# Kernel tuning notes

Hardware: AMD Instinct MI355X
Metric: run time of the kernel (lower is better)

## Reference

```python
import jax, jax.numpy as jnp
import numpy as np

WS = 7      # window size
SS = 3      # shift size = WS // 2
NH = 12     # num heads
EPS = 1e-5  # LayerNorm eps


def _ln(x, g, b):
    m = jnp.mean(x, axis=-1, keepdims=True)
    v = jnp.var(x, axis=-1, keepdims=True)
    return (x - m) * jax.lax.rsqrt(v + EPS) * g + b


def _rel_index(ws):
    # relative position index (N, N), N = ws*ws (static, numpy)
    coords = np.stack(np.meshgrid(np.arange(ws), np.arange(ws), indexing='ij')).reshape(2, -1)
    rel = (coords[:, :, None] - coords[:, None, :]).transpose(1, 2, 0).copy()
    rel[:, :, 0] += ws - 1
    rel[:, :, 1] += ws - 1
    rel[:, :, 0] *= 2 * ws - 1
    return rel.sum(-1)


def _attn_mask(H, W, ws, ss):
    # SW-MSA mask (nW, N, N): -100 where tokens come from different shifted regions
    img = np.zeros((H, W), np.float32)
    cnt = 0
    sls = (slice(0, -ws), slice(-ws, -ss), slice(-ss, None))
    for hs in sls:
        for wsl in sls:
            img[hs, wsl] = cnt
            cnt += 1
    win = img.reshape(H // ws, ws, W // ws, ws).transpose(0, 2, 1, 3).reshape(-1, ws * ws)
    d = win[:, None, :] - win[:, :, None]
    return np.where(d != 0, -100.0, 0.0).astype(np.float32)


def _forward(x, rel_bias_table, qkv_w, qkv_b, proj_w, proj_b,
             norm1_w, norm1_b, norm2_w, norm2_b,
             mlp_w1, mlp_b1, mlp_w2, mlp_b2, h, w):
    B, L, C = x.shape
    ws, ss, nH = WS, SS, NH
    hd = C // nH
    N = ws * ws
    scale = hd ** -0.5
    nWh, nWw = h // ws, w // ws
    nW = nWh * nWw

    shortcut = x
    y = _ln(x, norm1_w, norm1_b).reshape(B, h, w, C)
    # cyclic shift (SW-MSA)
    y = jnp.roll(y, (-ss, -ss), axis=(1, 2))
    # window partition -> (B*nW, N, C)
    y = y.reshape(B, nWh, ws, nWw, ws, C).transpose(0, 1, 3, 2, 4, 5).reshape(-1, N, C)

    qkv = (y @ qkv_w + qkv_b).reshape(-1, N, 3, nH, hd).transpose(2, 0, 3, 1, 4)
    q, k, v = qkv[0] * scale, qkv[1], qkv[2]  # (Bw, nH, N, hd)

    attn = jnp.einsum('bhnd,bhmd->bhnm', q, k)  # (Bw, nH, N, N)
    # learned relative position bias
    idx = jnp.asarray(_rel_index(ws))  # (N, N)
    bias = rel_bias_table[idx].transpose(2, 0, 1)[None]  # (1, nH, N, N)
    attn = attn + bias
    # shifted-window mask
    mask = jnp.asarray(_attn_mask(h, w, ws, ss))  # (nW, N, N)
    attn = attn.reshape(B, nW, nH, N, N) + mask[None, :, None]
    attn = jax.nn.softmax(attn.reshape(-1, nH, N, N), axis=-1)

    out = jnp.einsum('bhnm,bhmd->bhnd', attn, v).transpose(0, 2, 1, 3).reshape(-1, N, C)
    out = out @ proj_w + proj_b
    # window reverse + un-shift
    out = out.reshape(B, nWh, nWw, ws, ws, C).transpose(0, 1, 3, 2, 4, 5).reshape(B, h, w, C)
    out = jnp.roll(out, (ss, ss), axis=(1, 2)).reshape(B, L, C)

    x = shortcut + out
    y2 = _ln(x, norm2_w, norm2_b)
    mlp = jax.nn.gelu(y2 @ mlp_w1 + mlp_b1, approximate=False) @ mlp_w2 + mlp_b2
    return x + mlp


def setup_inputs() -> dict:
    key = jax.random.key(0)
    ks = jax.random.split(key, 8)
    B, H, W, C = 32, 56, 56, 384
    hid = int(C * 4.0)
    ws, nH = WS, NH
    inp = {
        'x': jax.random.normal(ks[0], (B, H * W, C), jnp.float32),
        'rel_bias_table': 0.02 * jax.random.normal(ks[1], ((2 * ws - 1) * (2 * ws - 1), nH), jnp.float32),
        'qkv_w': 0.02 * jax.random.normal(ks[2], (C, 3 * C), jnp.float32),
        'qkv_b': jnp.zeros((3 * C,), jnp.float32),
        'proj_w': 0.02 * jax.random.normal(ks[3], (C, C), jnp.float32),
        'proj_b': jnp.zeros((C,), jnp.float32),
        'norm1_w': jnp.ones((C,), jnp.float32),
        'norm1_b': jnp.zeros((C,), jnp.float32),
        'norm2_w': jnp.ones((C,), jnp.float32),
        'norm2_b': jnp.zeros((C,), jnp.float32),
        'mlp_w1': 0.02 * jax.random.normal(ks[4], (C, hid), jnp.float32),
        'mlp_b1': jnp.zeros((hid,), jnp.float32),
        'mlp_w2': 0.02 * jax.random.normal(ks[5], (hid, C), jnp.float32),
        'mlp_b2': jnp.zeros((C,), jnp.float32),
        'h': H,
        'w': W,
    }
    return inp


def reference(x, rel_bias_table, qkv_w, qkv_b, proj_w, proj_b,
              norm1_w, norm1_b, norm2_w, norm2_b,
              mlp_w1, mlp_b1, mlp_w2, mlp_b2, h, w):
    return _forward(x, rel_bias_table, qkv_w, qkv_b, proj_w, proj_b,
                    norm1_w, norm1_b, norm2_w, norm2_b,
                    mlp_w1, mlp_b1, mlp_w2, mlp_b2, h, w)
```

## Files before the change

### kernel.cpp

```cpp
#include <hip/hip_runtime.h>

typedef unsigned short u16;
typedef unsigned int u32;
typedef short s8v __attribute__((ext_vector_type(8)));
typedef float f4 __attribute__((ext_vector_type(4)));

#define GL16(g, l) __builtin_amdgcn_global_load_lds((const __attribute__((address_space(1))) u32*)(g), (__attribute__((address_space(3))) u32*)(l), 16, 0, 0)

__device__ __forceinline__ u16 f2bf(float f){
  u32 u = __builtin_bit_cast(u32, f);
  u32 r = u + 0x7fffu + ((u >> 16) & 1u);
  return (u16)(r >> 16);
}
__device__ __forceinline__ float bf2f(u16 u){
  u32 x = ((u32)u) << 16;
  return __builtin_bit_cast(float, x);
}

__device__ __forceinline__ u32 pk_bf16(float lo, float hi){
  u32 r;
  asm("v_cvt_pk_bf16_f32 %0, %1, %2" : "=v"(r) : "v"(lo), "v"(hi));
  return r;
}

__device__ __forceinline__ float gelu_f(float x){
  float y = fabsf(x) * 0.70710678118654752f;
  float t = __builtin_amdgcn_rcpf(1.f + 0.3275911f*y);
  float p = ((((1.061405429f*t - 1.453152027f)*t + 1.421413741f)*t - 0.284496736f)*t + 0.254829592f)*t;
  float er = 1.f - p*__expf(-y*y);
  er = copysignf(er, x);
  return 0.5f*x*(1.f + er);
}

__device__ __forceinline__ int win_to_src(int orow){
  int wi = orow / 49;
  int n  = orow - wi*49;
  int b  = wi >> 6;
  int wq = wi & 63;
  int wh = wq >> 3, ww = wq & 7;
  int r = n / 7, c = n - r*7;
  int hh = wh*7 + r + 3; if (hh >= 56) hh -= 56;
  int wp = ww*7 + c + 3; if (wp >= 56) wp -= 56;
  return (b*56 + hh)*56 + wp;
}

__global__ void sentinel_kernel(float* o){ o[0] = 1.0e9f; }

__global__ void transpose_cast(const float* __restrict__ in, u16* __restrict__ out,
                               int K, int N, float scale, int scale_lim){
  __shared__ float tile[16][17];
  int kb = blockIdx.x*16, nb = blockIdx.y*16;
  int tx = threadIdx.x, ty = threadIdx.y;
  int k = kb + ty, n = nb + tx;
  tile[ty][tx] = (k < K && n < N) ? in[(size_t)k*N + n] : 0.f;
  __syncthreads();
  int on = nb + ty, ok = kb + tx;
  if (on < N && ok < K){
    float v = tile[tx][ty];
    if (on < scale_lim) v *= scale;
    out[(size_t)on*K + ok] = f2bf(v);
  }
}

__global__ void scale_bias(const float* __restrict__ in, float* __restrict__ out,
                           int n, float s, int lim){
  int i = blockIdx.x*256 + threadIdx.x;
  if (i < n) out[i] = in[i] * (i < lim ? s : 1.f);
}

__global__ void build_biasmask(const float* __restrict__ table, u16* __restrict__ bm){
  int wq = blockIdx.x, h = blockIdx.y;
  int wh = wq >> 3, ww = wq & 7;
  u16* o = bm + (size_t)(wq*12 + h) * 4096;
  for (int i = threadIdx.x; i < 4096; i += 256){
    int m = i >> 6, n = i & 63;
    float v;
    if (m < 49 && n < 49){
      int rm = m/7, cm = m - rm*7;
      int rn = n/7, cn = n - rn*7;
      int idx = (rm - rn + 6)*13 + (cm - cn + 6);
      v = table[idx*12 + h];
      int ym = wh*7 + rm, xm = ww*7 + cm;
      int yn = wh*7 + rn, xn = ww*7 + cn;
      int lm = (ym < 49 ? 0 : (ym < 53 ? 1 : 2))*3 + (xm < 49 ? 0 : (xm < 53 ? 1 : 2));
      int ln = (yn < 49 ? 0 : (yn < 53 ? 1 : 2))*3 + (xn < 49 ? 0 : (xn < 53 ? 1 : 2));
      if (lm != ln) v += -100.f;
    } else {
      v = -1e9f;
    }
    o[i] = f2bf(v);
  }
}

template<bool GATHER>
__global__ __launch_bounds__(256) void ln_kernel(const float* __restrict__ x,
    const float* __restrict__ g, const float* __restrict__ b,
    u16* __restrict__ y, int nrows)
{
  int row = blockIdx.x*4 + (threadIdx.x >> 6);
  int lane = threadIdx.x & 63;
  if (row >= nrows) return;
  int src = GATHER ? win_to_src(row) : row;
  const float* xr = x + (size_t)src*384;
  float v[6];
  float s = 0.f, s2 = 0.f;
  #pragma unroll
  for (int p = 0; p < 3; p++){
    float2 t = *(const float2*)(xr + p*128 + lane*2);
    v[p*2] = t.x; v[p*2+1] = t.y;
    s += t.x + t.y; s2 += t.x*t.x + t.y*t.y;
  }
  #pragma unroll
  for (int off = 32; off; off >>= 1){
    s  += __shfl_xor(s,  off);
    s2 += __shfl_xor(s2, off);
  }
  float mean = s * (1.f/384.f);
  float var  = s2 * (1.f/384.f) - mean*mean;
  float rs   = rsqrtf(var + 1e-5f);
  u16* yr = y + (size_t)row*384;
  #pragma unroll
  for (int p = 0; p < 3; p++){
    int c = p*128 + lane*2;
    float a0 = (v[p*2]   - mean)*rs*g[c]   + b[c];
    float a1 = (v[p*2+1] - mean)*rs*g[c+1] + b[c+1];
    *(u32*)(yr + c) = pk_bf16(a0, a1);
  }
}

template<int MODE>
__global__ __launch_bounds__(512, 4) void gemm_bf16(
    const u16* __restrict__ A, const u16* __restrict__ Bt,
    const float* __restrict__ bias, const float* __restrict__ resid,
    void* __restrict__ outp, int K, int N, int gn)
{
  __shared__ u16 smem[36864];
  const int tid  = threadIdx.x;
  const int lane = tid & 63, wv = tid >> 6;
  const int wm = wv >> 1, wn = wv & 1;
  const int l15 = lane & 15, lhi = lane >> 4;
  const int key = (l15 >> 1) & 3;

  int total = gridDim.x;
  int flat  = blockIdx.x;
  int swz   = flat;
  if ((total & 7) == 0){
    int cpx = total >> 3;
    swz = (flat & 7)*cpx + (flat >> 3);
  }
  int bm = swz / gn, bn = swz - bm*gn;
  const size_t m0 = (size_t)bm * 256;
  const int n0 = bn * 128;

  f4 acc[4][4] = {};

  const int c0 = tid, c1 = 512 + tid;
  const u16* sA0 = A + (m0 + (size_t)(c0 >> 2))*K + ((c0 & 3) ^ ((c0 >> 3) & 3))*8;
  const u16* sA1 = A + (m0 + (size_t)(c1 >> 2))*K + ((c1 & 3) ^ ((c1 >> 3) & 3))*8;
  const u16* sB0 = Bt + ((size_t)n0 + (c0 >> 2))*K + ((c0 & 3) ^ ((c0 >> 3) & 3))*8;
  const int dA0 = (0   + wv*64)*8, dA1 = (512 + wv*64)*8;
  const int dB0 = dA0;

  int aoff[4], boff[4];
  #pragma unroll
  for (int mi = 0; mi < 4; mi++)
    aoff[mi] = (wm*64 + mi*16 + l15)*32 + (lhi ^ key)*8;
  #pragma unroll
  for (int ni = 0; ni < 4; ni++)
    boff[ni] = (wn*64 + ni*16 + l15)*32 + (lhi ^ key)*8;

  const int nk = K >> 5;

  GL16(sA0, &smem[0*8192 + dA0]); GL16(sA1, &smem[0*8192 + dA1]);
  GL16(sB0, &smem[24576 + 0*4096 + dB0]);
  GL16(sA0+32, &smem[1*8192 + dA0]); GL16(sA1+32, &smem[1*8192 + dA1]);
  GL16(sB0+32, &smem[24576 + 1*4096 + dB0]);
  sA0 += 64; sA1 += 64; sB0 += 64;

  int kt = 0;
  #define KSTEP(BUF_CUR, BUF_N2)                                               \
  {                                                                            \
    if (kt + 1 < nk) { asm volatile("s_waitcnt vmcnt(3)" ::: "memory"); }      \
    else             { asm volatile("s_waitcnt vmcnt(0)" ::: "memory"); }      \
    asm volatile("s_waitcnt lgkmcnt(0)" ::: "memory");                         \
    __builtin_amdgcn_s_barrier();                                              \
    if (kt + 2 < nk){                                                          \
      GL16(sA0, &smem[(BUF_N2)*8192 + dA0]);                                   \
      GL16(sA1, &smem[(BUF_N2)*8192 + dA1]);                                   \
      GL16(sB0, &smem[24576 + (BUF_N2)*4096 + dB0]);                           \
      sA0 += 32; sA1 += 32; sB0 += 32;                                         \
    }                                                                          \
    s8v a[4], bb[4];                                                           \
    _Pragma("unroll")                                                          \
    for (int mi = 0; mi < 4; mi++)                                             \
      a[mi] = *(const s8v*)&smem[(BUF_CUR)*8192 + aoff[mi]];                   \
    _Pragma("unroll")                                                          \
    for (int ni = 0; ni < 4; ni++)                                             \
      bb[ni] = *(const s8v*)&smem[24576 + (BUF_CUR)*4096 + boff[ni]];          \
    __builtin_amdgcn_s_setprio(1);                                             \
    _Pragma("unroll")                                                          \
    for (int mi = 0; mi < 4; mi++)                                             \
      _Pragma("unroll")                                                        \
      for (int ni = 0; ni < 4; ni++)                                           \
        acc[mi][ni] = __builtin_amdgcn_mfma_f32_16x16x32_bf16(                 \
            bb[ni], a[mi], acc[mi][ni], 0, 0, 0);                              \
    __builtin_amdgcn_s_setprio(0);                                             \
    kt++;                                                                      \
  }

  const int nIter = nk / 3;
  for (int it3 = 0; it3 < nIter; it3++){
    KSTEP(0, 2)
    KSTEP(1, 0)
    KSTEP(2, 1)
  }
  #undef KSTEP

  if constexpr (MODE == 0 || MODE == 2){
    asm volatile("s_waitcnt lgkmcnt(0)" ::: "memory");
    __builtin_amdgcn_s_barrier();
    u16* tile = smem;
    #pragma unroll
    for (int mi = 0; mi < 4; mi++){
      int ml = wm*64 + mi*16 + l15;
      #pragma unroll
      for (int ni = 0; ni < 4; ni++){
        int nl = wn*64 + ni*16 + lhi*4;
        f4 v = acc[mi][ni];
        float4 b4 = *(const float4*)(bias + n0 + nl);
        v[0] += b4.x; v[1] += b4.y; v[2] += b4.z; v[3] += b4.w;
        u32 p0, p1;
        if constexpr (MODE == 2){
          p0 = pk_bf16(gelu_f(v[0]), gelu_f(v[1]));
          p1 = pk_bf16(gelu_f(v[2]), gelu_f(v[3]));
        } else {
          p0 = pk_bf16(v[0], v[1]);
          p1 = pk_bf16(v[2], v[3]);
        }
        *(u32*)&tile[ml*136 + nl]     = p0;
        *(u32*)&tile[ml*136 + nl + 2] = p1;
      }
    }
    __syncthreads();
    int rr = tid >> 4;
    int cc = (tid & 15) * 8;
    #pragma unroll
    for (int pass = 0; pass < 8; pass++){
      int row = rr + pass*32;
      uint4 val = *(const uint4*)&tile[row*136 + cc];
      *(uint4*)((u16*)outp + ((size_t)((int)m0 + row))*N + n0 + cc) = val;
    }
  } else {
    #pragma unroll
    for (int mi = 0; mi < 4; mi++){
      int m = (int)m0 + wm*64 + mi*16 + l15;
      int src = 0;
      if constexpr (MODE == 1) src = win_to_src(m);
      #pragma unroll
      for (int ni = 0; ni < 4; ni++){
        int n = n0 + wn*64 + ni*16 + lhi*4;
        f4 v = acc[mi][ni];
        float4 b4 = *(const float4*)(bias + n);
        v[0] += b4.x; v[1] += b4.y; v[2] += b4.z; v[3] += b4.w;
        if constexpr (MODE == 1){
          const float4 r4 = *(const float4*)(resid + (size_t)src*384 + n);
          float4 o4; o4.x = v[0]+r4.x; o4.y = v[1]+r4.y; o4.z = v[2]+r4.z; o4.w = v[3]+r4.w;
          *(float4*)((float*)outp + (size_t)src*384 + n) = o4;
        } else {
          float4* o = (float4*)((float*)outp + (size_t)m*N + n);
          float4 c4 = *o;
          c4.x += v[0]; c4.y += v[1]; c4.z += v[2]; c4.w += v[3];
          *o = c4;
        }
      }
    }
  }
}

__global__ __launch_bounds__(256) void attn_kernel(
    const u16* __restrict__ qkv, const u16* __restrict__ bm, u16* __restrict__ ao)
{
  const int wi = blockIdx.x;
  const int hg = blockIdx.y;
  const int wv = threadIdx.x >> 6, lane = threadIdx.x & 63;
  const int h = hg*4 + wv;
  const int l15 = lane & 15, lhi = lane >> 4;
  const int wq = wi & 63;

  __shared__ u16 Plds[4][64*72];
  __shared__ u16 Vlds[4][32*72];

  const size_t base = (size_t)wi * 49 * 1152;
  s8v z8 = (s8v)0;

  #pragma unroll
  for (int i = 0; i < 4; i++){
    int n  = i*16 + (lane >> 2);
    int d8 = (lane & 3)*8;
    s8v v = (n < 49) ? *(const s8v*)&qkv[base + (size_t)n*1152 + 768 + h*32 + d8] : z8;
    #pragma unroll
    for (int j = 0; j < 8; j++)
      Vlds[wv][(d8 + j)*72 + n] = (u16)v[j];
  }

  s8v aQ[4], bK[4];
  #pragma unroll
  for (int mi = 0; mi < 4; mi++){
    int rowq = mi*16 + l15;
    aQ[mi] = (rowq < 49) ? *(const s8v*)&qkv[base + (size_t)rowq*1152 +   0 + h*32 + lhi*8] : z8;
    bK[mi] = (rowq < 49) ? *(const s8v*)&qkv[base + (size_t)rowq*1152 + 384 + h*32 + lhi*8] : z8;
  }
  f4 zf = {0.f, 0.f, 0.f, 0.f};
  f4 s[4][4];
  __builtin_amdgcn_s_setprio(1);
  #pragma unroll
  for (int mi = 0; mi < 4; mi++)
    #pragma unroll
    for (int ni = 0; ni < 4; ni++)
      s[mi][ni] = __builtin_amdgcn_mfma_f32_16x16x32_bf16(aQ[mi], bK[ni], zf, 0, 0, 0);
  __builtin_amdgcn_s_setprio(0);

  const u16* bmp = bm + (size_t)(wq*12 + h) * 4096;
  #pragma unroll
  for (int mi = 0; mi < 4; mi++)
    #pragma unroll
    for (int ni = 0; ni < 4; ni++)
      #pragma unroll
      for (int r = 0; r < 4; r++){
        int m = mi*16 + lhi*4 + r, n = ni*16 + l15;
        s[mi][ni][r] += bf2f(bmp[m*64 + n]);
      }

  #pragma unroll
  for (int mi = 0; mi < 4; mi++){
    #pragma unroll
    for (int r = 0; r < 4; r++){
      float mx = fmaxf(fmaxf(s[mi][0][r], s[mi][1][r]), fmaxf(s[mi][2][r], s[mi][3][r]));
      mx = fmaxf(mx, __shfl_xor(mx, 1));
      mx = fmaxf(mx, __shfl_xor(mx, 2));
      mx = fmaxf(mx, __shfl_xor(mx, 4));
      mx = fmaxf(mx, __shfl_xor(mx, 8));
      float sum = 0.f;
      #pragma unroll
      for (int ni = 0; ni < 4; ni++){
        float p = __expf(s[mi][ni][r] - mx);
        s[mi][ni][r] = p; sum += p;
      }
      sum += __shfl_xor(sum, 1);
      sum += __shfl_xor(sum, 2);
      sum += __shfl_xor(sum, 4);
      sum += __shfl_xor(sum, 8);
      float inv = 1.f / sum;
      #pragma unroll
      for (int ni = 0; ni < 4; ni++) s[mi][ni][r] *= inv;
    }
  }

  #pragma unroll
  for (int mi = 0; mi < 4; mi++)
    #pragma unroll
    for (int ni = 0; ni < 4; ni++)
      #pragma unroll
      for (int r = 0; r < 4; r++){
        int m = mi*16 + lhi*4 + r, n = ni*16 + l15;
        Plds[wv][m*72 + n] = f2bf(s[mi][ni][r]);
      }
  __syncthreads();

  f4 o[4][2] = {};
  #pragma unroll
  for (int ks = 0; ks < 2; ks++){
    s8v aP[4], bV[2];
    #pragma unroll
    for (int mi = 0; mi < 4; mi++)
      aP[mi] = *(const s8v*)&Plds[wv][(mi*16 + l15)*72 + ks*32 + lhi*8];
    #pragma unroll
    for (int di = 0; di < 2; di++)
      bV[di] = *(const s8v*)&Vlds[wv][(di*16 + l15)*72 + ks*32 + lhi*8];
    __builtin_amdgcn_s_setprio(1);
    #pragma unroll
    for (int mi = 0; mi < 4; mi++)
      #pragma unroll
      for (int di = 0; di < 2; di++)
        o[mi][di] = __builtin_amdgcn_mfma_f32_16x16x32_bf16(aP[mi], bV[di], o[mi][di], 0, 0, 0);
    __builtin_amdgcn_s_setprio(0);
  }

  #pragma unroll
  for (int mi = 0; mi < 4; mi++)
    #pragma unroll
    for (int di = 0; di < 2; di++)
      #pragma unroll
      for (int r = 0; r < 4; r++){
        int m = mi*16 + lhi*4 + r;
        if (m < 49){
          int d = di*16 + l15;
          ao[((size_t)wi*49 + m)*384 + h*32 + d] = f2bf(o[mi][di][r]);
        }
      }
}

extern "C" void kernel_launch(void* const* d_in, const int* in_sizes, int n_in,
                              void* d_out, int out_size, void* d_ws, size_t ws_size,
                              hipStream_t stream)
{
  const float* x      = (const float*)d_in[0];
  const float* table  = (const float*)d_in[1];
  const float* qkv_w  = (const float*)d_in[2];
  const float* qkv_b  = (const float*)d_in[3];
  const float* proj_w = (const float*)d_in[4];
  const float* proj_b = (const float*)d_in[5];
  const float* n1w    = (const float*)d_in[6];
  const float* n1b    = (const float*)d_in[7];
  const float* n2w    = (const float*)d_in[8];
  const float* n2b    = (const float*)d_in[9];
  const float* w1     = (const float*)d_in[10];
  const float* b1     = (const float*)d_in[11];
  const float* w2     = (const float*)d_in[12];
  const float* b2     = (const float*)d_in[13];
  float* out = (float*)d_out;

  const size_t M = 100352;
  const float SC = 0.17677669529663689f;

  const size_t R1 = M * 1536 * 2;
  const size_t R2 = M * 384 * 2;
  const size_t R3 = (size_t)64*12*64*64*2;
  const size_t WT = (size_t)(1152*384 + 384*384 + 1536*384 + 384*1536) * 2;
  const size_t BB = 1152 * 4;
  const size_t needed = R1 + R2 + R3 + WT + BB;
  if (ws_size < needed){
    sentinel_kernel<<<1, 1, 0, stream>>>(out);
    return;
  }

  char* p = (char*)d_ws;
  u16*   qkvbuf = (u16*)p;
  u16*   ybuf   = (u16*)(p + R1);
  u16*   bmbuf  = (u16*)(p + R1 + R2);
  u16*   qkvT   = (u16*)(p + R1 + R2 + R3);
  u16*   projT  = qkvT  + (size_t)1152*384;
  u16*   w1T    = projT + (size_t)384*384;
  u16*   w2T    = w1T   + (size_t)1536*384;
  float* qkvb_s = (float*)(p + R1 + R2 + R3 + WT);

  transpose_cast<<<dim3(24, 72),  dim3(16,16), 0, stream>>>(qkv_w,  qkvT, 384, 1152, SC, 384);
  transpose_cast<<<dim3(24, 24),  dim3(16,16), 0, stream>>>(proj_w, projT, 384, 384, 1.f, 0);
  transpose_cast<<<dim3(24, 96),  dim3(16,16), 0, stream>>>(w1,     w1T,  384, 1536, 1.f, 0);
  transpose_cast<<<dim3(96, 24),  dim3(16,16), 0, stream>>>(w2,     w2T,  1536, 384, 1.f, 0);
  scale_bias<<<5, 256, 0, stream>>>(qkv_b, qkvb_s, 1152, SC, 384);
  build_biasmask<<<dim3(64, 12), 256, 0, stream>>>(table, bmbuf);

  ln_kernel<true><<<M/4, 256, 0, stream>>>(x, n1w, n1b, ybuf, (int)M);

  gemm_bf16<0><<<392*9, 512, 0, stream>>>(ybuf, qkvT, qkvb_s, nullptr, qkvbuf, 384, 1152, 9);

  attn_kernel<<<dim3(2048, 3), 256, 0, stream>>>(qkvbuf, bmbuf, ybuf);

  gemm_bf16<1><<<392*3, 512, 0, stream>>>(ybuf, projT, proj_b, x, out, 384, 384, 3);

  ln_kernel<false><<<M/4, 256, 0, stream>>>(out, n2w, n2b, ybuf, (int)M);

  gemm_bf16<2><<<392*12, 512, 0, stream>>>(ybuf, w1T, b1, nullptr, qkvbuf, 384, 1536, 12);

  gemm_bf16<3><<<392*3, 512, 0, stream>>>(qkvbuf, w2T, b2, nullptr, out, 1536, 384, 3);
}
```

Before: 874.5 us.

## Fuse MLP fc1+GELU+fc2 into one kernel keeping hidden activations in LDS

Replaces the separate fc1 (GELU, bf16 hidden write) and fc2 (accumulate into output) GEMM launches with a single fused kernel per 128-row tile. The A tile is loaded once into LDS, hidden chunks of 64 columns are computed, passed through GELU and staged in swizzled LDS, then immediately consumed by fc2 into register accumulators. This removes the round trip of the large hidden tensor through global memory and one launch. In exchange, weights are read straight from global memory without LDS staging, the grid is much smaller with heavy register use, and each hidden chunk needs a barrier, so per-block latency and occupancy may suffer.

```diff
diff --git a/kernel.cpp b/kernel.cpp
--- a/kernel.cpp
+++ b/kernel.cpp
@@ -216,7 +216,7 @@
   }
   #undef KSTEP
 
-  if constexpr (MODE == 0 || MODE == 2){
+  if constexpr (MODE == 0){
     asm volatile("s_waitcnt lgkmcnt(0)" ::: "memory");
     __builtin_amdgcn_s_barrier();
     u16* tile = smem;
@@ -229,14 +229,8 @@
         f4 v = acc[mi][ni];
         float4 b4 = *(const float4*)(bias + n0 + nl);
         v[0] += b4.x; v[1] += b4.y; v[2] += b4.z; v[3] += b4.w;
-        u32 p0, p1;
-        if constexpr (MODE == 2){
-          p0 = pk_bf16(gelu_f(v[0]), gelu_f(v[1]));
-          p1 = pk_bf16(gelu_f(v[2]), gelu_f(v[3]));
-        } else {
-          p0 = pk_bf16(v[0], v[1]);
-          p1 = pk_bf16(v[2], v[3]);
-        }
+        u32 p0 = pk_bf16(v[0], v[1]);
+        u32 p1 = pk_bf16(v[2], v[3]);
         *(u32*)&tile[ml*136 + nl]     = p0;
         *(u32*)&tile[ml*136 + nl + 2] = p1;
       }
@@ -254,25 +248,136 @@
     #pragma unroll
     for (int mi = 0; mi < 4; mi++){
       int m = (int)m0 + wm*64 + mi*16 + l15;
-      int src = 0;
-      if constexpr (MODE == 1) src = win_to_src(m);
+      int src = win_to_src(m);
       #pragma unroll
       for (int ni = 0; ni < 4; ni++){
         int n = n0 + wn*64 + ni*16 + lhi*4;
         f4 v = acc[mi][ni];
         float4 b4 = *(const float4*)(bias + n);
-        v[0] += b4.x; v[1] += b4.y; v[2] += b4.z; v[3] += b4.w;
-        if constexpr (MODE == 1){
-          const float4 r4 = *(const float4*)(resid + (size_t)src*384 + n);
-          float4 o4; o4.x = v[0]+r4.x; o4.y = v[1]+r4.y; o4.z = v[2]+r4.z; o4.w = v[3]+r4.w;
-          *(float4*)((float*)outp + (size_t)src*384 + n) = o4;
-        } else {
-          float4* o = (float4*)((float*)outp + (size_t)m*N + n);
-          float4 c4 = *o;
-          c4.x += v[0]; c4.y += v[1]; c4.z += v[2]; c4.w += v[3];
-          *o = c4;
-        }
-      }
+        const float4 r4 = *(const float4*)(resid + (size_t)src*384 + n);
+        float4 o4; o4.x = v[0]+b4.x+r4.x; o4.y = v[1]+b4.y+r4.y;
+        o4.z = v[2]+b4.z+r4.z; o4.w = v[3]+b4.w+r4.w;
+        *(float4*)((float*)outp + (size_t)src*384 + n) = o4;
+      }
+    }
+  }
+}
+
+__global__ __launch_bounds__(512, 2) void fused_mlp(
+    const u16* __restrict__ A, const u16* __restrict__ w1T,
+    const u16* __restrict__ w2T, const float* __restrict__ b1,
+    const float* __restrict__ b2, float* __restrict__ outp)
+{
+  __shared__ u16 smem[65536];
+  const int tid = threadIdx.x;
+  const int lane = tid & 63, wv = tid >> 6;
+  const int wm = wv >> 2, wn = wv & 3;
+  const int wm1 = wv & 3, wn1 = wv >> 2;
+  const int l15 = lane & 15, lhi = lane >> 4;
+
+  int total = gridDim.x, flat = blockIdx.x, swz = flat;
+  if ((total & 7) == 0){ int cpx = total >> 3; swz = (flat & 7)*cpx + (flat >> 3); }
+  const size_t m0 = (size_t)swz * 128;
+
+  #pragma unroll
+  for (int it = 0; it < 12; it++){
+    int idx = it*512 + tid;
+    int row = idx / 48, g = idx - row*48;
+    const u16* gp = A + (m0 + (size_t)row)*384 + (size_t)(g ^ (row & 7))*8;
+    GL16(gp, &smem[(it*512 + wv*64)*8]);
+  }
+  asm volatile("s_waitcnt vmcnt(0)" ::: "memory");
+  __builtin_amdgcn_s_barrier();
+
+  f4 oacc[4][6] = {};
+
+  auto chunk = [&](int hbase, u16* Hc){
+    f4 acc1[2][2] = {};
+    #pragma unroll
+    for (int ks = 0; ks < 12; ks++){
+      s8v wf[2], af[2];
+      #pragma unroll
+      for (int nj = 0; nj < 2; nj++){
+        int n = hbase + wn1*32 + nj*16 + l15;
+        wf[nj] = *(const s8v*)&w1T[(size_t)n*384 + ks*32 + lhi*8];
+      }
+      #pragma unroll
+      for (int mi = 0; mi < 2; mi++){
+        int m = wm1*32 + mi*16 + l15;
+        int gk = (ks*4 + lhi) ^ (m & 7);
+        af[mi] = *(const s8v*)&smem[m*384 + gk*8];
+      }
+      __builtin_amdgcn_s_setprio(1);
+      #pragma unroll
+      for (int mi = 0; mi < 2; mi++)
+        #pragma unroll
+        for (int nj = 0; nj < 2; nj++)
+          acc1[mi][nj] = __builtin_amdgcn_mfma_f32_16x16x32_bf16(
+              wf[nj], af[mi], acc1[mi][nj], 0, 0, 0);
+      __builtin_amdgcn_s_setprio(0);
+    }
+    #pragma unroll
+    for (int mi = 0; mi < 2; mi++){
+      int m = wm1*32 + mi*16 + l15;
+      #pragma unroll
+      for (int nj = 0; nj < 2; nj++){
+        int h = wn1*32 + nj*16 + lhi*4;
+        f4 v = acc1[mi][nj];
+        float4 b4 = *(const float4*)(b1 + hbase + h);
+        v[0]+=b4.x; v[1]+=b4.y; v[2]+=b4.z; v[3]+=b4.w;
+        u32 p0 = pk_bf16(gelu_f(v[0]), gelu_f(v[1]));
+        u32 p1 = pk_bf16(gelu_f(v[2]), gelu_f(v[3]));
+        int gh = (h >> 3) ^ (m & 7);
+        u32* dst = (u32*)&Hc[m*64 + gh*8 + (h & 7)];
+        dst[0] = p0; dst[1] = p1;
+      }
+    }
+    asm volatile("s_waitcnt lgkmcnt(0)" ::: "memory");
+    __builtin_amdgcn_s_barrier();
+
+    #pragma unroll
+    for (int ks = 0; ks < 2; ks++){
+      s8v a2[4], w2f[6];
+      #pragma unroll
+      for (int nj = 0; nj < 6; nj++){
+        int n = wn*96 + nj*16 + l15;
+        w2f[nj] = *(const s8v*)&w2T[(size_t)n*1536 + hbase + ks*32 + lhi*8];
+      }
+      #pragma unroll
+      for (int mi = 0; mi < 4; mi++){
+        int m = wm*64 + mi*16 + l15;
+        int gk = (ks*4 + lhi) ^ (m & 7);
+        a2[mi] = *(const s8v*)&Hc[m*64 + gk*8];
+      }
+      __builtin_amdgcn_s_setprio(1);
+      #pragma unroll
+      for (int mi = 0; mi < 4; mi++)
+        #pragma unroll
+        for (int nj = 0; nj < 6; nj++)
+          oacc[mi][nj] = __builtin_amdgcn_mfma_f32_16x16x32_bf16(
+              w2f[nj], a2[mi], oacc[mi][nj], 0, 0, 0);
+      __builtin_amdgcn_s_setprio(0);
+    }
+  };
+
+  for (int hp = 0; hp < 12; hp++){
+    chunk(hp*128,      &smem[49152]);
+    chunk(hp*128 + 64, &smem[57344]);
+  }
+
+  #pragma unroll
+  for (int mi = 0; mi < 4; mi++){
+    int m = (int)m0 + wm*64 + mi*16 + l15;
+    #pragma unroll
+    for (int nj = 0; nj < 6; nj++){
+      int n = wn*96 + nj*16 + lhi*4;
+      f4 v = oacc[mi][nj];
+      float4 b4 = *(const float4*)(b2 + n);
+      float4* o = (float4*)(outp + (size_t)m*384 + n);
+      float4 c4 = *o;
+      c4.x += v[0]+b4.x; c4.y += v[1]+b4.y;
+      c4.z += v[2]+b4.z; c4.w += v[3]+b4.w;
+      *o = c4;
     }
   }
 }
@@ -461,7 +566,5 @@
 
   ln_kernel<false><<<M/4, 256, 0, stream>>>(out, n2w, n2b, ybuf, (int)M);
 
-  gemm_bf16<2><<<392*12, 512, 0, stream>>>(ybuf, w1T, b1, nullptr, qkvbuf, 384, 1536, 12);
-
-  gemm_bf16<3><<<392*3, 512, 0, stream>>>(qkvbuf, w2T, b2, nullptr, out, 1536, 384, 3);
-}
+  fused_mlp<<<784, 512, 0, stream>>>(ybuf, w1T, w2T, b1, b2, out);
+}
```

Result: slower. 1.450 ms (+65.9%).

## Specialize GEMM warps into dedicated load producers and MFMA consumers

Applied to the files above, without the earlier changes.

Adds two producer wavefronts per GEMM block (640 threads) that issue all global-to-LDS loads, while the eight original wavefronts only read LDS and run MFMAs. This aims to take load issue and address arithmetic off the compute waves so loads overlap better with matrix math. It raises threads per block and register pressure under a tighter launch bound (640,5). Producers wait on vmcnt(12) while consumers wait on lgkmcnt, so correctness depends on barrier ordering with the global_load_lds path.

```diff
diff --git a/kernel.cpp b/kernel.cpp
--- a/kernel.cpp
+++ b/kernel.cpp
@@ -129,7 +129,7 @@
 }
 
 template<int MODE>
-__global__ __launch_bounds__(512, 4) void gemm_bf16(
+__global__ __launch_bounds__(640, 5) void gemm_bf16(
     const u16* __restrict__ A, const u16* __restrict__ Bt,
     const float* __restrict__ bias, const float* __restrict__ resid,
     void* __restrict__ outp, int K, int N, int gn)
@@ -137,6 +137,7 @@
   __shared__ u16 smem[36864];
   const int tid  = threadIdx.x;
   const int lane = tid & 63, wv = tid >> 6;
+  const bool producer = (wv >= 8);
   const int wm = wv >> 1, wn = wv & 1;
   const int l15 = lane & 15, lhi = lane >> 4;
   const int key = (l15 >> 1) & 3;
@@ -154,12 +155,39 @@
 
   f4 acc[4][4] = {};
 
-  const int c0 = tid, c1 = 512 + tid;
-  const u16* sA0 = A + (m0 + (size_t)(c0 >> 2))*K + ((c0 & 3) ^ ((c0 >> 3) & 3))*8;
-  const u16* sA1 = A + (m0 + (size_t)(c1 >> 2))*K + ((c1 & 3) ^ ((c1 >> 3) & 3))*8;
-  const u16* sB0 = Bt + ((size_t)n0 + (c0 >> 2))*K + ((c0 & 3) ^ ((c0 >> 3) & 3))*8;
-  const int dA0 = (0   + wv*64)*8, dA1 = (512 + wv*64)*8;
-  const int dB0 = dA0;
+  const int p = wv - 8;
+  const u16* spA[8]; const u16* spB[4];
+  int dA[8], dB[4];
+  if (producer){
+    #pragma unroll
+    for (int it = 0; it < 8; it++){
+      int c = (it*2 + p)*64 + lane;
+      int row = c >> 2;
+      int col = ((c & 3) ^ ((c >> 3) & 3)) * 8;
+      spA[it] = A + (m0 + (size_t)row)*K + col;
+      dA[it] = (it*2 + p)*512;
+    }
+    #pragma unroll
+    for (int it = 0; it < 4; it++){
+      int c = (it*2 + p)*64 + lane;
+      int row = c >> 2;
+      int col = ((c & 3) ^ ((c >> 3) & 3)) * 8;
+      spB[it] = Bt + ((size_t)n0 + row)*K + col;
+      dB[it] = (it*2 + p)*512;
+    }
+  }
+
+  #define STAGEP(BUF)                                                          \
+  {                                                                            \
+    _Pragma("unroll")                                                          \
+    for (int it = 0; it < 8; it++) GL16(spA[it], &smem[(BUF)*8192 + dA[it]]);  \
+    _Pragma("unroll")                                                          \
+    for (int it = 0; it < 4; it++) GL16(spB[it], &smem[24576 + (BUF)*4096 + dB[it]]); \
+    _Pragma("unroll")                                                          \
+    for (int it = 0; it < 8; it++) spA[it] += 32;                              \
+    _Pragma("unroll")                                                          \
+    for (int it = 0; it < 4; it++) spB[it] += 32;                              \
+  }
 
   int aoff[4], boff[4];
   #pragma unroll
@@ -171,40 +199,40 @@
 
   const int nk = K >> 5;
 
-  GL16(sA0, &smem[0*8192 + dA0]); GL16(sA1, &smem[0*8192 + dA1]);
-  GL16(sB0, &smem[24576 + 0*4096 + dB0]);
-  GL16(sA0+32, &smem[1*8192 + dA0]); GL16(sA1+32, &smem[1*8192 + dA1]);
-  GL16(sB0+32, &smem[24576 + 1*4096 + dB0]);
-  sA0 += 64; sA1 += 64; sB0 += 64;
+  if (producer){
+    STAGEP(0)
+    STAGEP(1)
+  }
 
   int kt = 0;
   #define KSTEP(BUF_CUR, BUF_N2)                                               \
   {                                                                            \
-    if (kt + 1 < nk) { asm volatile("s_waitcnt vmcnt(3)" ::: "memory"); }      \
-    else             { asm volatile("s_waitcnt vmcnt(0)" ::: "memory"); }      \
-    asm volatile("s_waitcnt lgkmcnt(0)" ::: "memory");                         \
+    if (producer){                                                             \
+      if (kt + 1 < nk) { asm volatile("s_waitcnt vmcnt(12)" ::: "memory"); }   \
+      else             { asm volatile("s_waitcnt vmcnt(0)" ::: "memory"); }    \
+    } else {                                                                   \
+      asm volatile("s_waitcnt lgkmcnt(0)" ::: "memory");                       \
+    }                                                                          \
     __builtin_amdgcn_s_barrier();                                              \
-    if (kt + 2 < nk){                                                          \
-      GL16(sA0, &smem[(BUF_N2)*8192 + dA0]);                                   \
-      GL16(sA1, &smem[(BUF_N2)*8192 + dA1]);                                   \
-      GL16(sB0, &smem[24576 + (BUF_N2)*4096 + dB0]);                           \
-      sA0 += 32; sA1 += 32; sB0 += 32;                                         \
-    }                                                                          \
-    s8v a[4], bb[4];                                                           \
-    _Pragma("unroll")                                                          \
-    for (int mi = 0; mi < 4; mi++)                                             \
-      a[mi] = *(const s8v*)&smem[(BUF_CUR)*8192 + aoff[mi]];                   \
-    _Pragma("unroll")                                                          \
-    for (int ni = 0; ni < 4; ni++)                                             \
-      bb[ni] = *(const s8v*)&smem[24576 + (BUF_CUR)*4096 + boff[ni]];          \
-    __builtin_amdgcn_s_setprio(1);                                             \
-    _Pragma("unroll")                                                          \
-    for (int mi = 0; mi < 4; mi++)                                             \
+    if (producer){                                                             \
+      if (kt + 2 < nk){ STAGEP(BUF_N2) }                                       \
+    } else {                                                                   \
+      s8v a[4], bb[4];                                                         \
+      _Pragma("unroll")                                                        \
+      for (int mi = 0; mi < 4; mi++)                                           \
+        a[mi] = *(const s8v*)&smem[(BUF_CUR)*8192 + aoff[mi]];                 \
       _Pragma("unroll")                                                        \
       for (int ni = 0; ni < 4; ni++)                                           \
-        acc[mi][ni] = __builtin_amdgcn_mfma_f32_16x16x32_bf16(                 \
-            bb[ni], a[mi], acc[mi][ni], 0, 0, 0);                              \
-    __builtin_amdgcn_s_setprio(0);                                             \
+        bb[ni] = *(const s8v*)&smem[24576 + (BUF_CUR)*4096 + boff[ni]];        \
+      __builtin_amdgcn_s_setprio(1);                                           \
+      _Pragma("unroll")                                                        \
+      for (int mi = 0; mi < 4; mi++)                                           \
+        _Pragma("unroll")                                                      \
+        for (int ni = 0; ni < 4; ni++)                                         \
+          acc[mi][ni] = __builtin_amdgcn_mfma_f32_16x16x32_bf16(               \
+              bb[ni], a[mi], acc[mi][ni], 0, 0, 0);                            \
+      __builtin_amdgcn_s_setprio(0);                                           \
+    }                                                                          \
     kt++;                                                                      \
   }
 
@@ -215,62 +243,69 @@
     KSTEP(2, 1)
   }
   #undef KSTEP
+  #undef STAGEP
 
   if constexpr (MODE == 0 || MODE == 2){
     asm volatile("s_waitcnt lgkmcnt(0)" ::: "memory");
     __builtin_amdgcn_s_barrier();
     u16* tile = smem;
-    #pragma unroll
-    for (int mi = 0; mi < 4; mi++){
-      int ml = wm*64 + mi*16 + l15;
-      #pragma unroll
-      for (int ni = 0; ni < 4; ni++){
-        int nl = wn*64 + ni*16 + lhi*4;
-        f4 v = acc[mi][ni];
-        float4 b4 = *(const float4*)(bias + n0 + nl);
-        v[0] += b4.x; v[1] += b4.y; v[2] += b4.z; v[3] += b4.w;
-        u32 p0, p1;
-        if constexpr (MODE == 2){
-          p0 = pk_bf16(gelu_f(v[0]), gelu_f(v[1]));
-          p1 = pk_bf16(gelu_f(v[2]), gelu_f(v[3]));
-        } else {
-          p0 = pk_bf16(v[0], v[1]);
-          p1 = pk_bf16(v[2], v[3]);
+    if (!producer){
+      #pragma unroll
+      for (int mi = 0; mi < 4; mi++){
+        int ml = wm*64 + mi*16 + l15;
+        #pragma unroll
+        for (int ni = 0; ni < 4; ni++){
+          int nl = wn*64 + ni*16 + lhi*4;
+          f4 v = acc[mi][ni];
+          float4 b4 = *(const float4*)(bias + n0 + nl);
+          v[0] += b4.x; v[1] += b4.y; v[2] += b4.z; v[3] += b4.w;
+          u32 p0, p1;
+          if constexpr (MODE == 2){
+            p0 = pk_bf16(gelu_f(v[0]), gelu_f(v[1]));
+            p1 = pk_bf16(gelu_f(v[2]), gelu_f(v[3]));
+          } else {
+            p0 = pk_bf16(v[0], v[1]);
+            p1 = pk_bf16(v[2], v[3]);
+          }
+          *(u32*)&tile[ml*136 + nl]     = p0;
+          *(u32*)&tile[ml*136 + nl + 2] = p1;
         }
-        *(u32*)&tile[ml*136 + nl]     = p0;
-        *(u32*)&tile[ml*136 + nl + 2] = p1;
       }
     }
     __syncthreads();
-    int rr = tid >> 4;
-    int cc = (tid & 15) * 8;
-    #pragma unroll
-    for (int pass = 0; pass < 8; pass++){
-      int row = rr + pass*32;
-      uint4 val = *(const uint4*)&tile[row*136 + cc];
-      *(uint4*)((u16*)outp + ((size_t)((int)m0 + row))*N + n0 + cc) = val;
+    if (tid < 512){
+      int rr = tid >> 4;
+      int cc = (tid & 15) * 8;
+      #pragma unroll
+      for (int pass = 0; pass < 8; pass++){
+        int row = rr + pass*32;
+        uint4 val = *(const uint4*)&tile[row*136 + cc];
+        *(uint4*)((u16*)outp + ((size_t)((int)m0 + row))*N + n0 + cc) = val;
+      }
     }
   } else {
-    #pragma unroll
-    for (int mi = 0; mi < 4; mi++){
-      int m = (int)m0 + wm*64 + mi*16 + l15;
-      int src = 0;
-      if constexpr (MODE == 1) src = win_to_src(m);
-      #pragma unroll
-      for (int ni = 0; ni < 4; ni++){
-        int n = n0 + wn*64 + ni*16 + lhi*4;
-        f4 v = acc[mi][ni];
-        float4 b4 = *(const float4*)(bias + n);
-        v[0] += b4.x; v[1] += b4.y; v[2] += b4.z; v[3] += b4.w;
-        if constexpr (MODE == 1){
-          const float4 r4 = *(const float4*)(resid + (size_t)src*384 + n);
-          float4 o4; o4.x = v[0]+r4.x; o4.y = v[1]+r4.y; o4.z = v[2]+r4.z; o4.w = v[3]+r4.w;
-          *(float4*)((float*)outp + (size_t)src*384 + n) = o4;
-        } else {
-          float4* o = (float4*)((float*)outp + (size_t)m*N + n);
-          float4 c4 = *o;
-          c4.x += v[0]; c4.y += v[1]; c4.z += v[2]; c4.w += v[3];
-          *o = c4;
+    if (!producer){
+      #pragma unroll
+      for (int mi = 0; mi < 4; mi++){
+        int m = (int)m0 + wm*64 + mi*16 + l15;
+        int src = 0;
+        if constexpr (MODE == 1) src = win_to_src(m);
+        #pragma unroll
+        for (int ni = 0; ni < 4; ni++){
+          int n = n0 + wn*64 + ni*16 + lhi*4;
+          f4 v = acc[mi][ni];
+          float4 b4 = *(const float4*)(bias + n);
+          v[0] += b4.x; v[1] += b4.y; v[2] += b4.z; v[3] += b4.w;
+          if constexpr (MODE == 1){
+            const float4 r4 = *(const float4*)(resid + (size_t)src*384 + n);
+            float4 o4; o4.x = v[0]+r4.x; o4.y = v[1]+r4.y; o4.z = v[2]+r4.z; o4.w = v[3]+r4.w;
+            *(float4*)((float*)outp + (size_t)src*384 + n) = o4;
+          } else {
+            float4* o = (float4*)((float*)outp + (size_t)m*N + n);
+            float4 c4 = *o;
+            c4.x += v[0]; c4.y += v[1]; c4.z += v[2]; c4.w += v[3];
+            *o = c4;
+          }
         }
       }
     }
@@ -453,15 +488,15 @@
 
   ln_kernel<true><<<M/4, 256, 0, stream>>>(x, n1w, n1b, ybuf, (int)M);
 
-  gemm_bf16<0><<<392*9, 512, 0, stream>>>(ybuf, qkvT, qkvb_s, nullptr, qkvbuf, 384, 1152, 9);
+  gemm_bf16<0><<<392*9, 640, 0, stream>>>(ybuf, qkvT, qkvb_s, nullptr, qkvbuf, 384, 1152, 9);
 
   attn_kernel<<<dim3(2048, 3), 256, 0, stream>>>(qkvbuf, bmbuf, ybuf);
 
-  gemm_bf16<1><<<392*3, 512, 0, stream>>>(ybuf, projT, proj_b, x, out, 384, 384, 3);
+  gemm_bf16<1><<<392*3, 640, 0, stream>>>(ybuf, projT, proj_b, x, out, 384, 384, 3);
 
   ln_kernel<false><<<M/4, 256, 0, stream>>>(out, n2w, n2b, ybuf, (int)M);
 
-  gemm_bf16<2><<<392*12, 512, 0, stream>>>(ybuf, w1T, b1, nullptr, qkvbuf, 384, 1536, 12);
-
-  gemm_bf16<3><<<392*3, 512, 0, stream>>>(qkvbuf, w2T, b2, nullptr, out, 1536, 384, 3);
-}
+  gemm_bf16<2><<<392*12, 640, 0, stream>>>(ybuf, w1T, b1, nullptr, qkvbuf, 384, 1536, 12);
+
+  gemm_bf16<3><<<392*3, 640, 0, stream>>>(qkvbuf, w2T, b2, nullptr, out, 1536, 384, 3);
+}
```

Result: slower. 2.700 ms (+208.7%).
